# Performance work log

Hardware: AMD Instinct MI355X
Metric: run time of the kernel (lower is better)

## Reference

```python
import math
import jax, jax.numpy as jnp
import numpy as np

B, H, D, N, M = 4, 8, 64, 8192, 256
EPS = 1e-6


def sample_orthogonal_random_vectors(num_rows, num_cols, seed=0):
    """Faithful port of FavorAttention.sample_orthogonal_random_vectors."""
    rng = np.random.default_rng(seed)
    num_blocks = math.ceil(num_rows / num_cols)
    unstructured = rng.standard_normal((num_blocks, num_cols, num_cols)).astype(np.float32)
    norm = np.linalg.norm(unstructured, axis=-1).reshape(-1, 1)
    q, _ = np.linalg.qr(unstructured)                 # reduced QR per block
    q = np.transpose(q, (0, 2, 1)).reshape(-1, num_cols)
    q = q[:num_rows, :] * norm[:num_rows, :]
    return jnp.asarray(q, dtype=jnp.float32)


def setup_inputs() -> dict:
    key = jax.random.key(0)
    kq, kk, kv = jax.random.split(key, 3)
    return {
        "query": jax.random.normal(kq, (B, H, D, N), dtype=jnp.float32),
        "key": jax.random.normal(kk, (B, H, D, N), dtype=jnp.float32),
        "value": jax.random.normal(kv, (B, H, D, N), dtype=jnp.float32),
        "projection_matrix": sample_orthogonal_random_vectors(M, D),
    }


def randomized_kernel(x, proj, is_query, eps=EPS):
    """FAVOR+ positive softmax features. x: [B,H,D,N] -> phi: [B,H,M,N]."""
    d = x.shape[2]
    data_normalizer = d ** -0.25
    ratio = proj.shape[0] ** -0.5
    # projected: [B,H,M,N]
    u = jnp.einsum('md,bhdn->bhmn', proj, x) * data_normalizer
    # ||x||^2 / (2*sqrt(d)) per token: [B,H,1,N]
    diag = jnp.sum(x * x, axis=2, keepdims=True) * (data_normalizer ** 2) * 0.5
    if is_query:
        stab = jnp.max(u, axis=2, keepdims=True)            # per-token max over features
    else:
        stab = jnp.max(u, axis=(2, 3), keepdims=True)       # global max per (b,h)
    return ratio * (jnp.exp(u - diag - stab) + eps)


def reference(query, key, value, projection_matrix):
    q_phi = randomized_kernel(query, projection_matrix, is_query=True)    # [B,H,M,N]
    k_phi = randomized_kernel(key, projection_matrix, is_query=False)     # [B,H,M,N]
    # kv = key @ value^T over sequence: [B,H,M,D]
    kv = jnp.einsum('bhmn,bhdn->bhmd', k_phi, value)
    key_norm = jnp.sum(k_phi, axis=3)                                     # [B,H,M]
    out = jnp.einsum('bhmn,bhmd->bhnd', q_phi, kv)                        # [B,H,N,D]
    out_norm = jnp.einsum('bhmn,bhm->bhn', q_phi, key_norm)[..., None]    # [B,H,N,1]
    out = out / out_norm
    return jnp.swapaxes(out, 2, 3)                                        # [B,H,D,N]


if __name__ == '__main__':
    o = reference(**setup_inputs())
    print(o.shape, o.dtype)
```

## Files before the change

kernel.cpp:

```cpp
#include <hip/hip_runtime.h>


typedef short s16x8 __attribute__((ext_vector_type(8)));
typedef float f32x4 __attribute__((ext_vector_type(4)));

#define Dv 64
#define Nv 8192
#define Mv 256
#define BHv 32
#define SPL 16
#define NSPL (Nv / SPL)
#define NCH (NSPL / 64)

#define DNRM 0.3535533905932738f
#define EPSV 1e-6f

#define OFF_DIAGK 0
#define OFF_MAXP (BHv * Nv)
#define OFF_STAB (OFF_MAXP + BHv * SPL)
#define OFF_KNP (OFF_STAB + BHv)
#define OFF_KNF (OFF_KNP + BHv * SPL * Mv)
#define OFF_KVP (OFF_KNF + BHv * Mv)
#define OFF_KVT (OFF_KVP + BHv * SPL * Mv * Dv)

__device__ __forceinline__ unsigned short f2b(float x) {
    return __builtin_bit_cast(unsigned short, (__bf16)x);
}

__device__ __forceinline__ s16x8 load_pfrag(const float* __restrict__ proj, int m,
                                            int kc, int q) {
    const float* p = proj + m * 64 + kc * 32 + q * 8;
    s16x8 r;
#pragma unroll
    for (int j = 0; j < 8; ++j) r[j] = (short)f2b(p[j]);
    return r;
}

__global__ __launch_bounds__(256, 2) void favor_kmax(const float* __restrict__ key,
                                                     const float* __restrict__ proj,
                                                     float* __restrict__ ws) {
    __shared__ __align__(16) unsigned short KT[64][72];
    __shared__ float dred[16][64];
    __shared__ float red[4];
    const int tid = threadIdx.x;
    const int w = tid >> 6, l = tid & 63, c = l & 15, q = l >> 4;
    const int g = tid >> 4, cs = tid & 15;
    const int s = blockIdx.x, bh = blockIdx.y;
    const float* kp = key + (size_t)bh * Dv * Nv;
    float* dgw = ws + OFF_DIAGK + bh * Nv;

    s16x8 P[4][2];
#pragma unroll
    for (int mt = 0; mt < 4; ++mt)
#pragma unroll
        for (int kc = 0; kc < 2; ++kc)
            P[mt][kc] = load_pfrag(proj, (4 * w + mt) * 16 + c, kc, q);

    float vmax = -3.4e38f;
    for (int ch = 0; ch < NCH; ++ch) {
        const int n0 = s * NSPL + ch * 64;
        if (ch) __syncthreads();
        float4 kk[4];
#pragma unroll
        for (int di = 0; di < 4; ++di)
            kk[di] = *(const float4*)&kp[(4 * g + di) * Nv + n0 + 4 * cs];
#pragma unroll
        for (int j = 0; j < 4; ++j) {
            const float v0 = ((const float*)&kk[0])[j];
            const float v1 = ((const float*)&kk[1])[j];
            const float v2 = ((const float*)&kk[2])[j];
            const float v3 = ((const float*)&kk[3])[j];
            *(short4*)&KT[4 * cs + j][4 * g] =
                make_short4((short)f2b(v0), (short)f2b(v1), (short)f2b(v2),
                            (short)f2b(v3));
            dred[g][4 * cs + j] = (v0 * v0 + v1 * v1) + (v2 * v2 + v3 * v3);
        }
        __syncthreads();
        if (tid < 64) {
            float dsum = 0.f;
#pragma unroll
            for (int gg = 0; gg < 16; ++gg) dsum += dred[gg][tid];
            dgw[n0 + tid] = dsum * 0.0625f;
        }
#pragma unroll
        for (int nt = 0; nt < 4; ++nt) {
            const s16x8 a0 = *(const s16x8*)&KT[nt * 16 + c][q * 8];
            const s16x8 a1 = *(const s16x8*)&KT[nt * 16 + c][32 + q * 8];
#pragma unroll
            for (int mt = 0; mt < 4; ++mt) {
                f32x4 u = {0.f, 0.f, 0.f, 0.f};
                u = __builtin_amdgcn_mfma_f32_16x16x32_bf16(a0, P[mt][0], u, 0, 0, 0);
                u = __builtin_amdgcn_mfma_f32_16x16x32_bf16(a1, P[mt][1], u, 0, 0, 0);
                vmax = fmaxf(vmax, fmaxf(fmaxf(u[0], u[1]), fmaxf(u[2], u[3])));
            }
        }
    }
#pragma unroll
    for (int off = 1; off < 64; off <<= 1)
        vmax = fmaxf(vmax, __shfl_xor(vmax, off, 64));
    if (l == 0) red[w] = vmax;
    __syncthreads();
    if (tid == 0)
        ws[OFF_MAXP + bh * SPL + s] =
            fmaxf(fmaxf(red[0], red[1]), fmaxf(red[2], red[3]));
}

__global__ __launch_bounds__(256, 2) void favor_kv(const float* __restrict__ key,
                                                   const float* __restrict__ value,
                                                   const float* __restrict__ proj,
                                                   float* __restrict__ ws) {
    __shared__ __align__(16) unsigned short KT[64][72];
    __shared__ __align__(16) unsigned short VL[64][72];
    __shared__ __align__(16) unsigned short PH[256][40];
    const int tid = threadIdx.x;
    const int w = tid >> 6, l = tid & 63, c = l & 15, q = l >> 4;
    const int g = tid >> 4, cs = tid & 15;
    const int s = blockIdx.x, bh = blockIdx.y;
    const float* kp = key + (size_t)bh * Dv * Nv;
    const float* vp = value + (size_t)bh * Dv * Nv;
    const float* dgp = ws + OFF_DIAGK + bh * Nv;

    float stab;
    {
        const float* mp = ws + OFF_MAXP + bh * SPL;
        float r = mp[0];
#pragma unroll
        for (int s2 = 1; s2 < SPL; ++s2) r = fmaxf(r, mp[s2]);
        stab = r * DNRM;
    }

    s16x8 P[4][2];
#pragma unroll
    for (int mt = 0; mt < 4; ++mt)
#pragma unroll
        for (int kc = 0; kc < 2; ++kc)
            P[mt][kc] = load_pfrag(proj, (4 * w + mt) * 16 + c, kc, q);

    f32x4 kva[4][4];
#pragma unroll
    for (int mt = 0; mt < 4; ++mt)
#pragma unroll
        for (int dt = 0; dt < 4; ++dt) kva[mt][dt] = (f32x4){0.f, 0.f, 0.f, 0.f};
    float kn[4] = {0.f, 0.f, 0.f, 0.f};

    for (int ch = 0; ch < NCH; ++ch) {
        const int n0 = s * NSPL + ch * 64;
        if (ch) __syncthreads();
        {
            float4 kk[4], vv[4];
#pragma unroll
            for (int di = 0; di < 4; ++di) {
                kk[di] = *(const float4*)&kp[(4 * g + di) * Nv + n0 + 4 * cs];
                vv[di] = *(const float4*)&vp[(4 * g + di) * Nv + n0 + 4 * cs];
            }
#pragma unroll
            for (int j = 0; j < 4; ++j)
                *(short4*)&KT[4 * cs + j][4 * g] = make_short4(
                    (short)f2b(((const float*)&kk[0])[j]),
                    (short)f2b(((const float*)&kk[1])[j]),
                    (short)f2b(((const float*)&kk[2])[j]),
                    (short)f2b(((const float*)&kk[3])[j]));
#pragma unroll
            for (int di = 0; di < 4; ++di)
                *(short4*)&VL[4 * g + di][4 * cs] = make_short4(
                    (short)f2b(vv[di].x), (short)f2b(vv[di].y),
                    (short)f2b(vv[di].z), (short)f2b(vv[di].w));
        }
        __syncthreads();
#pragma unroll
        for (int h = 0; h < 2; ++h) {
#pragma unroll
            for (int nt2 = 0; nt2 < 2; ++nt2) {
                const int nt = 2 * h + nt2;
                const s16x8 a0 = *(const s16x8*)&KT[nt * 16 + c][q * 8];
                const s16x8 a1 = *(const s16x8*)&KT[nt * 16 + c][32 + q * 8];
                const float4 dg = *(const float4*)&dgp[n0 + nt * 16 + q * 4];
#pragma unroll
                for (int mt = 0; mt < 4; ++mt) {
                    f32x4 u = {0.f, 0.f, 0.f, 0.f};
                    u = __builtin_amdgcn_mfma_f32_16x16x32_bf16(a0, P[mt][0], u, 0, 0, 0);
                    u = __builtin_amdgcn_mfma_f32_16x16x32_bf16(a1, P[mt][1], u, 0, 0, 0);
                    const float e0 = __expf(u[0] * DNRM - dg.x - stab) + EPSV;
                    const float e1 = __expf(u[1] * DNRM - dg.y - stab) + EPSV;
                    const float e2 = __expf(u[2] * DNRM - dg.z - stab) + EPSV;
                    const float e3 = __expf(u[3] * DNRM - dg.w - stab) + EPSV;
                    kn[mt] += (e0 + e1) + (e2 + e3);
                    *(short4*)&PH[(4 * w + mt) * 16 + c][nt2 * 16 + q * 4] =
                        make_short4((short)f2b(e0), (short)f2b(e1),
                                    (short)f2b(e2), (short)f2b(e3));
                }
            }
            s16x8 bf[4];
#pragma unroll
            for (int dt = 0; dt < 4; ++dt)
                bf[dt] = *(const s16x8*)&VL[dt * 16 + c][h * 32 + q * 8];
#pragma unroll
            for (int mt = 0; mt < 4; ++mt) {
                const s16x8 a = *(const s16x8*)&PH[(4 * w + mt) * 16 + c][q * 8];
#pragma unroll
                for (int dt = 0; dt < 4; ++dt)
                    kva[mt][dt] = __builtin_amdgcn_mfma_f32_16x16x32_bf16(
                        a, bf[dt], kva[mt][dt], 0, 0, 0);
            }
        }
    }
    float* kvp = ws + OFF_KVP + (size_t)(bh * SPL + s) * Mv * Dv;
#pragma unroll
    for (int mt = 0; mt < 4; ++mt) {
        const int mrow = (4 * w + mt) * 16 + 4 * q;
#pragma unroll
        for (int dt = 0; dt < 4; ++dt) {
            const int dcol = dt * 16 + c;
#pragma unroll
            for (int r = 0; r < 4; ++r)
                kvp[(size_t)(mrow + r) * Dv + dcol] = kva[mt][dt][r];
        }
    }
#pragma unroll
    for (int mt = 0; mt < 4; ++mt) {
        kn[mt] += __shfl_xor(kn[mt], 16, 64);
        kn[mt] += __shfl_xor(kn[mt], 32, 64);
    }
    if (q == 0) {
        float* knp = ws + OFF_KNP + (bh * SPL + s) * Mv;
#pragma unroll
        for (int mt = 0; mt < 4; ++mt) knp[(4 * w + mt) * 16 + c] = kn[mt];
    }
}

__global__ __launch_bounds__(256) void favor_kvred(float* __restrict__ ws) {
    const int t = threadIdx.x, f = blockIdx.x, bh = blockIdx.y;
    const int flat = f * 1024 + t * 4;
    const int m = flat >> 6, d0 = flat & 63;
    float4 acc = make_float4(0.f, 0.f, 0.f, 0.f);
    for (int s = 0; s < SPL; ++s) {
        const float4 v =
            *(const float4*)&ws[OFF_KVP + ((size_t)(bh * SPL + s) << 14) + flat];
        acc.x += v.x; acc.y += v.y; acc.z += v.z; acc.w += v.w;
    }
    unsigned short* kvT = (unsigned short*)(ws + OFF_KVT);
    kvT[(bh * 64 + d0 + 0) * 256 + m] = f2b(acc.x);
    kvT[(bh * 64 + d0 + 1) * 256 + m] = f2b(acc.y);
    kvT[(bh * 64 + d0 + 2) * 256 + m] = f2b(acc.z);
    kvT[(bh * 64 + d0 + 3) * 256 + m] = f2b(acc.w);
    if (t < 16) {
        const int mm = f * 16 + t;
        float kk = 0.f;
        for (int s = 0; s < SPL; ++s)
            kk += ws[OFF_KNP + (bh * SPL + s) * Mv + mm];
        ws[OFF_KNF + bh * Mv + mm] = kk;
    }
}

__global__ __launch_bounds__(256, 2) void favor_out(const float* __restrict__ query,
                                                    const float* __restrict__ proj,
                                                    const float* __restrict__ ws,
                                                    float* __restrict__ out) {
    __shared__ __align__(16) unsigned short PHT[64][264];
    __shared__ float npart[4][64];
    __shared__ float knl[256];
    __shared__ float cw[4][64];
    __shared__ float stabl[64];
    __shared__ float dql[64];
    unsigned short (*QT)[72] = (unsigned short (*)[72]) & PHT[0][0];
    float (*dred)[64] = (float (*)[64])((char*)&PHT[0][0] + 9216);
    const int tid = threadIdx.x;
    const int w = tid >> 6, l = tid & 63, c = l & 15, q = l >> 4;
    const int g = tid >> 4, cs = tid & 15;
    const int nb = blockIdx.x, bh = blockIdx.y;
    const int n0 = nb * 64;
    const float* qp = query + (size_t)bh * Dv * Nv;
    const unsigned short* kvT =
        (const unsigned short*)(ws + OFF_KVT) + (size_t)bh * 64 * 256;

    {
        float4 qq[4];
#pragma unroll
        for (int di = 0; di < 4; ++di)
            qq[di] = *(const float4*)&qp[(4 * g + di) * Nv + n0 + 4 * cs];
#pragma unroll
        for (int j = 0; j < 4; ++j) {
            const float v0 = ((const float*)&qq[0])[j];
            const float v1 = ((const float*)&qq[1])[j];
            const float v2 = ((const float*)&qq[2])[j];
            const float v3 = ((const float*)&qq[3])[j];
            *(short4*)&QT[4 * cs + j][4 * g] =
                make_short4((short)f2b(v0), (short)f2b(v1), (short)f2b(v2),
                            (short)f2b(v3));
            dred[g][4 * cs + j] = (v0 * v0 + v1 * v1) + (v2 * v2 + v3 * v3);
        }
    }
    knl[tid] = ws[OFF_KNF + bh * Mv + tid];

    s16x8 P[4][2];
#pragma unroll
    for (int mt = 0; mt < 4; ++mt)
#pragma unroll
        for (int kc = 0; kc < 2; ++kc)
            P[mt][kc] = load_pfrag(proj, (4 * w + mt) * 16 + c, kc, q);
    __syncthreads();

    f32x4 u[4][4];
#pragma unroll
    for (int mt = 0; mt < 4; ++mt)
#pragma unroll
        for (int nt = 0; nt < 4; ++nt) u[mt][nt] = (f32x4){0.f, 0.f, 0.f, 0.f};
#pragma unroll
    for (int nt = 0; nt < 4; ++nt) {
        const s16x8 b0 = *(const s16x8*)&QT[nt * 16 + c][q * 8];
        const s16x8 b1 = *(const s16x8*)&QT[nt * 16 + c][32 + q * 8];
#pragma unroll
        for (int mt = 0; mt < 4; ++mt) {
            u[mt][nt] =
                __builtin_amdgcn_mfma_f32_16x16x32_bf16(P[mt][0], b0, u[mt][nt], 0, 0, 0);
            u[mt][nt] =
                __builtin_amdgcn_mfma_f32_16x16x32_bf16(P[mt][1], b1, u[mt][nt], 0, 0, 0);
        }
    }
#pragma unroll
    for (int nt = 0; nt < 4; ++nt) {
        float vm = -3.4e38f;
#pragma unroll
        for (int mt = 0; mt < 4; ++mt)
            vm = fmaxf(vm, fmaxf(fmaxf(u[mt][nt][0], u[mt][nt][1]),
                                 fmaxf(u[mt][nt][2], u[mt][nt][3])));
        vm = fmaxf(vm, __shfl_xor(vm, 16, 64));
        vm = fmaxf(vm, __shfl_xor(vm, 32, 64));
        if (q == 0) cw[w][nt * 16 + c] = vm;
    }
    __syncthreads();
    if (tid < 64) {
        stabl[tid] =
            fmaxf(fmaxf(cw[0][tid], cw[1][tid]), fmaxf(cw[2][tid], cw[3][tid]));
        float dsum = 0.f;
#pragma unroll
        for (int gg = 0; gg < 16; ++gg) dsum += dred[gg][tid];
        dql[tid] = dsum * 0.0625f;
    }
    __syncthreads();
#pragma unroll
    for (int nt = 0; nt < 4; ++nt) {
        const float sr = stabl[nt * 16 + c];
        const float dq = dql[nt * 16 + c];
        float np = 0.f;
#pragma unroll
        for (int mt = 0; mt < 4; ++mt) {
            const float e0 = __expf((u[mt][nt][0] - sr) * DNRM - dq) + EPSV;
            const float e1 = __expf((u[mt][nt][1] - sr) * DNRM - dq) + EPSV;
            const float e2 = __expf((u[mt][nt][2] - sr) * DNRM - dq) + EPSV;
            const float e3 = __expf((u[mt][nt][3] - sr) * DNRM - dq) + EPSV;
            const int mb = (4 * w + mt) * 16 + 4 * q;
            np += e0 * knl[mb] + e1 * knl[mb + 1] + e2 * knl[mb + 2] +
                  e3 * knl[mb + 3];
            *(short4*)&PHT[nt * 16 + c][mb] = make_short4(
                (short)f2b(e0), (short)f2b(e1), (short)f2b(e2), (short)f2b(e3));
        }
        np += __shfl_xor(np, 16, 64);
        np += __shfl_xor(np, 32, 64);
        if (q == 0) npart[w][nt * 16 + c] = np;
    }
    __syncthreads();
    f32x4 acc[4];
#pragma unroll
    for (int dt = 0; dt < 4; ++dt) acc[dt] = (f32x4){0.f, 0.f, 0.f, 0.f};
#pragma unroll
    for (int kc = 0; kc < 8; ++kc) {
        const s16x8 a = *(const s16x8*)&PHT[w * 16 + c][kc * 32 + q * 8];
#pragma unroll
        for (int dt = 0; dt < 4; ++dt) {
            const s16x8 b =
                *(const s16x8*)&kvT[(size_t)(dt * 16 + c) * 256 + kc * 32 + q * 8];
            acc[dt] = __builtin_amdgcn_mfma_f32_16x16x32_bf16(a, b, acc[dt], 0, 0, 0);
        }
    }
    __syncthreads();
    float* ot = (float*)&PHT[0][0];
    float rn[4];
#pragma unroll
    for (int r = 0; r < 4; ++r) {
        const int nl = w * 16 + 4 * q + r;
        rn[r] = 1.0f / ((npart[0][nl] + npart[1][nl]) +
                        (npart[2][nl] + npart[3][nl]));
    }
#pragma unroll
    for (int dt = 0; dt < 4; ++dt)
#pragma unroll
        for (int r = 0; r < 4; ++r)
            ot[(dt * 16 + c) * 68 + (w * 16 + 4 * q + r)] = acc[dt][r] * rn[r];
    __syncthreads();
    float* op = out + (size_t)bh * Dv * Nv;
    {
        const int d = tid >> 2, ng = (tid & 3) * 16;
#pragma unroll
        for (int i = 0; i < 4; ++i) {
            const float4 v = *(const float4*)&ot[d * 68 + ng + i * 4];
            *(float4*)&op[d * Nv + n0 + ng + i * 4] = v;
        }
    }
}

extern "C" void kernel_launch(void* const* d_in, const int* in_sizes, int n_in,
                              void* d_out, int out_size, void* d_ws, size_t ws_size,
                              hipStream_t stream) {
    const float* q = (const float*)d_in[0];
    const float* k = (const float*)d_in[1];
    const float* v = (const float*)d_in[2];
    const float* proj = (const float*)d_in[3];
    float* ws = (float*)d_ws;
    float* out = (float*)d_out;

    favor_kmax<<<dim3(SPL, 32), 256, 0, stream>>>(k, proj, ws);
    favor_kv<<<dim3(SPL, 32), 256, 0, stream>>>(k, v, proj, ws);
    favor_kvred<<<dim3(16, 32), 256, 0, stream>>>(ws);
    favor_out<<<dim3(Nv / 64, 32), 256, 0, stream>>>(q, proj, ws, out);
}
```

Measured before the change: 327.9 us.

## Fuse key max pass into kv kernel with online rescaling of partial sums

Removes the separate favor_kmax pass over the key tensor. favor_kv now tracks a running per-wave max, rescales its kv and key-norm accumulators when the max grows, and computes the key diag in shared memory. favor_kvred rescales each split's partials to the global max and adds the eps term analytically through per-d value sums. This saves a full read of the key and a launch, at the cost of extra reductions, syncs and exp rescaling inside the kv loop. Because the rescale factor differs per wave, rounding may differ slightly from the reference.

```diff
diff --git a/kernel.cpp b/kernel.cpp
--- a/kernel.cpp
+++ b/kernel.cpp
@@ -15,10 +15,9 @@
 #define DNRM 0.3535533905932738f
 #define EPSV 1e-6f
 
-#define OFF_DIAGK 0
-#define OFF_MAXP (BHv * Nv)
-#define OFF_STAB (OFF_MAXP + BHv * SPL)
-#define OFF_KNP (OFF_STAB + BHv)
+#define OFF_SGM 0
+#define OFF_SVP (OFF_SGM + BHv * SPL * 4)
+#define OFF_KNP (OFF_SVP + BHv * SPL * 64)
 #define OFF_KNF (OFF_KNP + BHv * SPL * Mv)
 #define OFF_KVP (OFF_KNF + BHv * Mv)
 #define OFF_KVT (OFF_KVP + BHv * SPL * Mv * Dv)
@@ -34,75 +33,6 @@
 #pragma unroll
     for (int j = 0; j < 8; ++j) r[j] = (short)f2b(p[j]);
     return r;
-}
-
-__global__ __launch_bounds__(256, 2) void favor_kmax(const float* __restrict__ key,
-                                                     const float* __restrict__ proj,
-                                                     float* __restrict__ ws) {
-    __shared__ __align__(16) unsigned short KT[64][72];
-    __shared__ float dred[16][64];
-    __shared__ float red[4];
-    const int tid = threadIdx.x;
-    const int w = tid >> 6, l = tid & 63, c = l & 15, q = l >> 4;
-    const int g = tid >> 4, cs = tid & 15;
-    const int s = blockIdx.x, bh = blockIdx.y;
-    const float* kp = key + (size_t)bh * Dv * Nv;
-    float* dgw = ws + OFF_DIAGK + bh * Nv;
-
-    s16x8 P[4][2];
-#pragma unroll
-    for (int mt = 0; mt < 4; ++mt)
-#pragma unroll
-        for (int kc = 0; kc < 2; ++kc)
-            P[mt][kc] = load_pfrag(proj, (4 * w + mt) * 16 + c, kc, q);
-
-    float vmax = -3.4e38f;
-    for (int ch = 0; ch < NCH; ++ch) {
-        const int n0 = s * NSPL + ch * 64;
-        if (ch) __syncthreads();
-        float4 kk[4];
-#pragma unroll
-        for (int di = 0; di < 4; ++di)
-            kk[di] = *(const float4*)&kp[(4 * g + di) * Nv + n0 + 4 * cs];
-#pragma unroll
-        for (int j = 0; j < 4; ++j) {
-            const float v0 = ((const float*)&kk[0])[j];
-            const float v1 = ((const float*)&kk[1])[j];
-            const float v2 = ((const float*)&kk[2])[j];
-            const float v3 = ((const float*)&kk[3])[j];
-            *(short4*)&KT[4 * cs + j][4 * g] =
-                make_short4((short)f2b(v0), (short)f2b(v1), (short)f2b(v2),
-                            (short)f2b(v3));
-            dred[g][4 * cs + j] = (v0 * v0 + v1 * v1) + (v2 * v2 + v3 * v3);
-        }
-        __syncthreads();
-        if (tid < 64) {
-            float dsum = 0.f;
-#pragma unroll
-            for (int gg = 0; gg < 16; ++gg) dsum += dred[gg][tid];
-            dgw[n0 + tid] = dsum * 0.0625f;
-        }
-#pragma unroll
-        for (int nt = 0; nt < 4; ++nt) {
-            const s16x8 a0 = *(const s16x8*)&KT[nt * 16 + c][q * 8];
-            const s16x8 a1 = *(const s16x8*)&KT[nt * 16 + c][32 + q * 8];
-#pragma unroll
-            for (int mt = 0; mt < 4; ++mt) {
-                f32x4 u = {0.f, 0.f, 0.f, 0.f};
-                u = __builtin_amdgcn_mfma_f32_16x16x32_bf16(a0, P[mt][0], u, 0, 0, 0);
-                u = __builtin_amdgcn_mfma_f32_16x16x32_bf16(a1, P[mt][1], u, 0, 0, 0);
-                vmax = fmaxf(vmax, fmaxf(fmaxf(u[0], u[1]), fmaxf(u[2], u[3])));
-            }
-        }
-    }
-#pragma unroll
-    for (int off = 1; off < 64; off <<= 1)
-        vmax = fmaxf(vmax, __shfl_xor(vmax, off, 64));
-    if (l == 0) red[w] = vmax;
-    __syncthreads();
-    if (tid == 0)
-        ws[OFF_MAXP + bh * SPL + s] =
-            fmaxf(fmaxf(red[0], red[1]), fmaxf(red[2], red[3]));
 }
 
 __global__ __launch_bounds__(256, 2) void favor_kv(const float* __restrict__ key,
@@ -112,22 +42,14 @@
     __shared__ __align__(16) unsigned short KT[64][72];
     __shared__ __align__(16) unsigned short VL[64][72];
     __shared__ __align__(16) unsigned short PH[256][40];
+    __shared__ __align__(16) float dred[16][64];
+    __shared__ __align__(16) float dgl[64];
     const int tid = threadIdx.x;
     const int w = tid >> 6, l = tid & 63, c = l & 15, q = l >> 4;
     const int g = tid >> 4, cs = tid & 15;
     const int s = blockIdx.x, bh = blockIdx.y;
     const float* kp = key + (size_t)bh * Dv * Nv;
     const float* vp = value + (size_t)bh * Dv * Nv;
-    const float* dgp = ws + OFF_DIAGK + bh * Nv;
-
-    float stab;
-    {
-        const float* mp = ws + OFF_MAXP + bh * SPL;
-        float r = mp[0];
-#pragma unroll
-        for (int s2 = 1; s2 < SPL; ++s2) r = fmaxf(r, mp[s2]);
-        stab = r * DNRM;
-    }
 
     s16x8 P[4][2];
 #pragma unroll
@@ -142,6 +64,8 @@
 #pragma unroll
         for (int dt = 0; dt < 4; ++dt) kva[mt][dt] = (f32x4){0.f, 0.f, 0.f, 0.f};
     float kn[4] = {0.f, 0.f, 0.f, 0.f};
+    float sv[4] = {0.f, 0.f, 0.f, 0.f};
+    float mx = -3.0e38f;
 
     for (int ch = 0; ch < NCH; ++ch) {
         const int n0 = s * NSPL + ch * 64;
@@ -154,36 +78,79 @@
                 vv[di] = *(const float4*)&vp[(4 * g + di) * Nv + n0 + 4 * cs];
             }
 #pragma unroll
-            for (int j = 0; j < 4; ++j)
-                *(short4*)&KT[4 * cs + j][4 * g] = make_short4(
-                    (short)f2b(((const float*)&kk[0])[j]),
-                    (short)f2b(((const float*)&kk[1])[j]),
-                    (short)f2b(((const float*)&kk[2])[j]),
-                    (short)f2b(((const float*)&kk[3])[j]));
-#pragma unroll
-            for (int di = 0; di < 4; ++di)
+            for (int j = 0; j < 4; ++j) {
+                const float k0 = ((const float*)&kk[0])[j];
+                const float k1 = ((const float*)&kk[1])[j];
+                const float k2 = ((const float*)&kk[2])[j];
+                const float k3 = ((const float*)&kk[3])[j];
+                *(short4*)&KT[4 * cs + j][4 * g] =
+                    make_short4((short)f2b(k0), (short)f2b(k1), (short)f2b(k2),
+                                (short)f2b(k3));
+                dred[g][4 * cs + j] = (k0 * k0 + k1 * k1) + (k2 * k2 + k3 * k3);
+            }
+#pragma unroll
+            for (int di = 0; di < 4; ++di) {
                 *(short4*)&VL[4 * g + di][4 * cs] = make_short4(
                     (short)f2b(vv[di].x), (short)f2b(vv[di].y),
                     (short)f2b(vv[di].z), (short)f2b(vv[di].w));
+                sv[di] += (vv[di].x + vv[di].y) + (vv[di].z + vv[di].w);
+            }
         }
         __syncthreads();
+        if (tid < 64) {
+            float ds = 0.f;
+#pragma unroll
+            for (int gg = 0; gg < 16; ++gg) ds += dred[gg][tid];
+            dgl[tid] = ds * 0.0625f;
+        }
+        __syncthreads();
 #pragma unroll
         for (int h = 0; h < 2; ++h) {
+            f32x4 u[4][2];
 #pragma unroll
             for (int nt2 = 0; nt2 < 2; ++nt2) {
                 const int nt = 2 * h + nt2;
                 const s16x8 a0 = *(const s16x8*)&KT[nt * 16 + c][q * 8];
                 const s16x8 a1 = *(const s16x8*)&KT[nt * 16 + c][32 + q * 8];
-                const float4 dg = *(const float4*)&dgp[n0 + nt * 16 + q * 4];
 #pragma unroll
                 for (int mt = 0; mt < 4; ++mt) {
-                    f32x4 u = {0.f, 0.f, 0.f, 0.f};
-                    u = __builtin_amdgcn_mfma_f32_16x16x32_bf16(a0, P[mt][0], u, 0, 0, 0);
-                    u = __builtin_amdgcn_mfma_f32_16x16x32_bf16(a1, P[mt][1], u, 0, 0, 0);
-                    const float e0 = __expf(u[0] * DNRM - dg.x - stab) + EPSV;
-                    const float e1 = __expf(u[1] * DNRM - dg.y - stab) + EPSV;
-                    const float e2 = __expf(u[2] * DNRM - dg.z - stab) + EPSV;
-                    const float e3 = __expf(u[3] * DNRM - dg.w - stab) + EPSV;
+                    f32x4 t = {0.f, 0.f, 0.f, 0.f};
+                    t = __builtin_amdgcn_mfma_f32_16x16x32_bf16(a0, P[mt][0], t, 0, 0, 0);
+                    t = __builtin_amdgcn_mfma_f32_16x16x32_bf16(a1, P[mt][1], t, 0, 0, 0);
+                    u[mt][nt2] = t;
+                }
+            }
+            float cm = -3.0e38f;
+#pragma unroll
+            for (int mt = 0; mt < 4; ++mt)
+#pragma unroll
+                for (int nt2 = 0; nt2 < 2; ++nt2)
+                    cm = fmaxf(cm, fmaxf(fmaxf(u[mt][nt2][0], u[mt][nt2][1]),
+                                         fmaxf(u[mt][nt2][2], u[mt][nt2][3])));
+            cm *= DNRM;
+#pragma unroll
+            for (int off = 1; off < 64; off <<= 1)
+                cm = fmaxf(cm, __shfl_xor(cm, off, 64));
+            if (cm > mx) {
+                const float al = __expf(mx - cm);
+#pragma unroll
+                for (int mt = 0; mt < 4; ++mt) {
+#pragma unroll
+                    for (int dt = 0; dt < 4; ++dt) kva[mt][dt] *= al;
+                    kn[mt] *= al;
+                }
+                mx = cm;
+            }
+#pragma unroll
+            for (int nt2 = 0; nt2 < 2; ++nt2) {
+                const int nt = 2 * h + nt2;
+                const float4 dg = *(const float4*)&dgl[nt * 16 + q * 4];
+#pragma unroll
+                for (int mt = 0; mt < 4; ++mt) {
+                    const float e0 = __expf(u[mt][nt2][0] * DNRM - dg.x - mx);
+                    const float e1 = __expf(u[mt][nt2][1] * DNRM - dg.y - mx);
+                    const float e2 = __expf(u[mt][nt2][2] * DNRM - dg.z - mx);
+                    const float e3 = __expf(u[mt][nt2][3] * DNRM - dg.w - mx);
                     kn[mt] += (e0 + e1) + (e2 + e3);
                     *(short4*)&PH[(4 * w + mt) * 16 + c][nt2 * 16 + q * 4] =
                         make_short4((short)f2b(e0), (short)f2b(e1),
@@ -226,18 +193,59 @@
 #pragma unroll
         for (int mt = 0; mt < 4; ++mt) knp[(4 * w + mt) * 16 + c] = kn[mt];
     }
+    if (l == 0) ws[OFF_SGM + (bh * SPL + s) * 4 + w] = mx;
+    __syncthreads();
+    float* sp = &dred[0][0];
+#pragma unroll
+    for (int di = 0; di < 4; ++di) sp[(4 * g + di) * 16 + cs] = sv[di];
+    __syncthreads();
+    if (tid < 64) {
+        float t2 = 0.f;
+#pragma unroll
+        for (int j = 0; j < 16; ++j) t2 += sp[tid * 16 + j];
+        ws[OFF_SVP + (bh * SPL + s) * 64 + tid] = t2;
+    }
 }
 
 __global__ __launch_bounds__(256) void favor_kvred(float* __restrict__ ws) {
+    __shared__ float sgl[64];
+    __shared__ float alph[SPL];
+    __shared__ float svl[64];
+    __shared__ float Gs;
     const int t = threadIdx.x, f = blockIdx.x, bh = blockIdx.y;
     const int flat = f * 1024 + t * 4;
     const int m = flat >> 6, d0 = flat & 63;
+    const int wgrp = f >> 2;
+    if (t < 64) {
+        const float v = ws[OFF_SGM + bh * 64 + t];
+        sgl[t] = v;
+        float gm = v;
+#pragma unroll
+        for (int off = 1; off < 64; off <<= 1)
+            gm = fmaxf(gm, __shfl_xor(gm, off, 64));
+        if (t == 0) Gs = gm;
+    } else if (t < 128) {
+        const int d = t - 64;
+        float x = 0.f;
+#pragma unroll
+        for (int s2 = 0; s2 < SPL; ++s2)
+            x += ws[OFF_SVP + (bh * SPL + s2) * 64 + d];
+        svl[d] = x;
+    }
+    __syncthreads();
+    if (t < SPL) alph[t] = __expf(sgl[t * 4 + wgrp] - Gs);
+    __syncthreads();
     float4 acc = make_float4(0.f, 0.f, 0.f, 0.f);
-    for (int s = 0; s < SPL; ++s) {
+    for (int s2 = 0; s2 < SPL; ++s2) {
+        const float a = alph[s2];
         const float4 v =
-            *(const float4*)&ws[OFF_KVP + ((size_t)(bh * SPL + s) << 14) + flat];
-        acc.x += v.x; acc.y += v.y; acc.z += v.z; acc.w += v.w;
-    }
+            *(const float4*)&ws[OFF_KVP + ((size_t)(bh * SPL + s2) << 14) + flat];
+        acc.x += a * v.x; acc.y += a * v.y; acc.z += a * v.z; acc.w += a * v.w;
+    }
+    acc.x += EPSV * svl[d0 + 0];
+    acc.y += EPSV * svl[d0 + 1];
+    acc.z += EPSV * svl[d0 + 2];
+    acc.w += EPSV * svl[d0 + 3];
     unsigned short* kvT = (unsigned short*)(ws + OFF_KVT);
     kvT[(bh * 64 + d0 + 0) * 256 + m] = f2b(acc.x);
     kvT[(bh * 64 + d0 + 1) * 256 + m] = f2b(acc.y);
@@ -246,9 +254,9 @@
     if (t < 16) {
         const int mm = f * 16 + t;
         float kk = 0.f;
-        for (int s = 0; s < SPL; ++s)
-            kk += ws[OFF_KNP + (bh * SPL + s) * Mv + mm];
-        ws[OFF_KNF + bh * Mv + mm] = kk;
+        for (int s2 = 0; s2 < SPL; ++s2)
+            kk += alph[s2] * ws[OFF_KNP + (bh * SPL + s2) * Mv + mm];
+        ws[OFF_KNF + bh * Mv + mm] = kk + EPSV * (float)Nv;
     }
 }
 
@@ -409,7 +417,6 @@
     float* ws = (float*)d_ws;
     float* out = (float*)d_out;
 
-    favor_kmax<<<dim3(SPL, 32), 256, 0, stream>>>(k, proj, ws);
     favor_kv<<<dim3(SPL, 32), 256, 0, stream>>>(k, v, proj, ws);
     favor_kvred<<<dim3(16, 32), 256, 0, stream>>>(ws);
     favor_out<<<dim3(Nv / 64, 32), 256, 0, stream>>>(q, proj, ws, out);
```

Result: no change. 321.6 us (-1.9%).
